# Kernel optimization log

Hardware: AMD Instinct MI355X
Metric: run time of the kernel (lower is better)

The kernel has to match this reference:

```python
import jax, jax.numpy as jnp
import numpy as np

BBOX_STD_DEV = jnp.array([0.1, 0.1, 0.2, 0.2], dtype=jnp.float32)
MIN_CONF = 0.15          # hardcoded in source (tf.where(probs >= 0.15))
NMS_THR = 0.3            # config.DETECTION_NMS_THRESHOLD
MAX_INST = 100           # config.DETECTION_MAX_INSTANCES
B, N = 8, 2048


def apply_box_deltas(boxes, deltas):
    # boxes: [N,4] (y1,x1,y2,x2); deltas: [N,4] (dy,dx,log dh,log dw)
    h = boxes[:, 2] - boxes[:, 0]
    w = boxes[:, 3] - boxes[:, 1]
    cy = boxes[:, 0] + 0.5 * h + deltas[:, 0] * h
    cx = boxes[:, 1] + 0.5 * w + deltas[:, 1] * w
    h = h * jnp.exp(deltas[:, 2])
    w = w * jnp.exp(deltas[:, 3])
    y1 = cy - 0.5 * h
    x1 = cx - 0.5 * w
    return jnp.stack([y1, x1, y1 + h, x1 + w], axis=1)


def clip_boxes(boxes, window):
    wy1, wx1, wy2, wx2 = window[0], window[1], window[2], window[3]
    y1 = jnp.clip(boxes[:, 0], wy1, wy2)
    x1 = jnp.clip(boxes[:, 1], wx1, wx2)
    y2 = jnp.clip(boxes[:, 2], wy1, wy2)
    x2 = jnp.clip(boxes[:, 3], wx1, wx2)
    return jnp.stack([y1, x1, y2, x2], axis=1)


def pairwise_iou(boxes):
    # boxes: [N,4] -> iou: [N,N]
    y1, x1, y2, x2 = boxes[:, 0], boxes[:, 1], boxes[:, 2], boxes[:, 3]
    area = (y2 - y1) * (x2 - x1)
    iy1 = jnp.maximum(y1[:, None], y1[None, :])
    ix1 = jnp.maximum(x1[:, None], x1[None, :])
    iy2 = jnp.minimum(y2[:, None], y2[None, :])
    ix2 = jnp.minimum(x2[:, None], x2[None, :])
    inter = jnp.maximum(iy2 - iy1, 0.0) * jnp.maximum(ix2 - ix1, 0.0)
    union = area[:, None] + area[None, :] - inter
    return inter / (union + 1e-8)


def refine_one(rois_i, probs_i, deltas_i, window_i):
    scores = probs_i[:, 0]
    boxes = clip_boxes(apply_box_deltas(rois_i, deltas_i * BBOX_STD_DEV), window_i)
    valid = scores >= MIN_CONF  # confidence filter (mask instead of gather)

    # sort by score descending; greedy NMS over sorted order
    order = jnp.argsort(-scores)
    sb, ss, sv = boxes[order], scores[order], valid[order]
    iou = pairwise_iou(sb)  # [N,N]
    idx = jnp.arange(N)

    def step(kept, xs):
        i, row, v = xs
        suppressed = jnp.any(kept & (idx < i) & (row > NMS_THR))
        return kept.at[i].set(v & ~suppressed), None

    kept, _ = jax.lax.scan(step, jnp.zeros((N,), dtype=bool), (idx, iou, sv))

    # top-k kept by score (already sorted desc, so top_k over masked scores)
    masked = jnp.where(kept, ss, -jnp.inf)
    _, top_i = jax.lax.top_k(masked, MAX_INST)
    ok = kept[top_i]
    det = jnp.concatenate([sb[top_i], ss[top_i][:, None]], axis=1)  # [MAX_INST,5]
    return jnp.where(ok[:, None], det, 0.0)  # zero-pad slots past num kept


def setup_inputs() -> dict:
    key = jax.random.key(0)
    k1, k2, k3 = jax.random.split(key, 3)
    # well-formed normalized rois: y1<y2, x1<x2
    yy = jnp.sort(jax.random.uniform(k1, (B, N, 2)), axis=-1)
    xx = jnp.sort(jax.random.uniform(jax.random.fold_in(k1, 1), (B, N, 2)), axis=-1)
    rois = jnp.stack([yy[..., 0], xx[..., 0], yy[..., 1], xx[..., 1]], axis=-1)
    bbox_scores = jax.random.uniform(k2, (B, N, 1), dtype=jnp.float32)
    deltas = jax.random.normal(k3, (B, N, 4), dtype=jnp.float32) * 0.1
    window = jnp.tile(jnp.array([[0.02, 0.02, 0.98, 0.98]], dtype=jnp.float32), (B, 1))
    return {"rois": rois, "bbox_scores": bbox_scores, "deltas": deltas, "window": window}


def reference(rois, bbox_scores, deltas, window):
    # -> [B, MAX_INST, 5] (y1,x1,y2,x2,score), normalized coords, zero padded
    return jax.vmap(refine_one)(rois, bbox_scores, deltas, window)
```

## Files before the change

kernel.cpp:

```cpp
#include <hip/hip_runtime.h>
#include <math.h>

#define NBOX 2048
#define NBATCH 8
#define MAX_INST 100
#define MIN_CONF 0.15f
#define NMS_THR 0.3f
#define BLOCK 512
#define NWAVE (BLOCK / 64)

typedef unsigned long long ull;

__device__ inline float4 decode_box(float4 r, float4 d,
                                    float wy1, float wx1, float wy2, float wx2) {
    float h  = __fsub_rn(r.z, r.x);
    float w  = __fsub_rn(r.w, r.y);
    float dy = __fmul_rn(d.x, 0.1f);
    float dx = __fmul_rn(d.y, 0.1f);
    float dh = __fmul_rn(d.z, 0.2f);
    float dw = __fmul_rn(d.w, 0.2f);
    float cy = __fadd_rn(__fadd_rn(r.x, __fmul_rn(0.5f, h)), __fmul_rn(dy, h));
    float cx = __fadd_rn(__fadd_rn(r.y, __fmul_rn(0.5f, w)), __fmul_rn(dx, w));
    float h2 = __fmul_rn(h, expf(dh));
    float w2 = __fmul_rn(w, expf(dw));
    float y1 = __fsub_rn(cy, __fmul_rn(0.5f, h2));
    float x1 = __fsub_rn(cx, __fmul_rn(0.5f, w2));
    float y2 = __fadd_rn(y1, h2);
    float x2 = __fadd_rn(x1, w2);
    float4 b;
    b.x = fminf(fmaxf(y1, wy1), wy2);
    b.y = fminf(fmaxf(x1, wx1), wx2);
    b.z = fminf(fmaxf(y2, wy1), wy2);
    b.w = fminf(fmaxf(x2, wx1), wx2);
    return b;
}

__device__ inline float iou_pair(float4 a, float4 b) {
    float areaA = __fmul_rn(__fsub_rn(a.z, a.x), __fsub_rn(a.w, a.y));
    float areaB = __fmul_rn(__fsub_rn(b.z, b.x), __fsub_rn(b.w, b.y));
    float iy1 = fmaxf(a.x, b.x);
    float ix1 = fmaxf(a.y, b.y);
    float iy2 = fminf(a.z, b.z);
    float ix2 = fminf(a.w, b.w);
    float ih = fmaxf(__fsub_rn(iy2, iy1), 0.0f);
    float iw = fmaxf(__fsub_rn(ix2, ix1), 0.0f);
    float inter = __fmul_rn(ih, iw);
    float uni = __fadd_rn(__fsub_rn(__fadd_rn(areaA, areaB), inter), 1e-8f);
    return __fdiv_rn(inter, uni);
}

__device__ inline ull shfl_xor64(ull x, int d) {
    unsigned lo = (unsigned)x, hi = (unsigned)(x >> 32);
    lo = __shfl_xor(lo, d);
    hi = __shfl_xor(hi, d);
    return ((ull)hi << 32) | lo;
}

__device__ inline ull shfl64(ull x, int src) {
    unsigned lo = (unsigned)x, hi = (unsigned)(x >> 32);
    lo = __shfl(lo, src);
    hi = __shfl(hi, src);
    return ((ull)hi << 32) | lo;
}

__device__ inline void cmpsel(ull& a, ull& b, bool takeMinA) {
    ull mn = a < b ? a : b;
    ull mx = a < b ? b : a;
    a = takeMinA ? mn : mx;
    b = takeMinA ? mx : mn;
}

__global__ __launch_bounds__(BLOCK)
void detect_refine_kernel(const float* __restrict__ rois,
                          const float* __restrict__ scores_in,
                          const float* __restrict__ deltas,
                          const float* __restrict__ window,
                          float* __restrict__ out) {
    const int b    = blockIdx.x;
    const int tid  = threadIdx.x;
    const int lane = tid & 63;
    const int wid  = tid >> 6;

    __shared__ ull    keys[NBOX];
    __shared__ float4 sboxes[NBOX];
    __shared__ float  sscores[NBOX];
    __shared__ ull    masks[64];
    __shared__ ull    dead8[NWAVE];
    __shared__ float4 s_keptbox[MAX_INST];
    __shared__ int    s_keptslot[64];
    __shared__ int    s_m;
    __shared__ ull    s_alive;

    const float wy1 = window[b * 4 + 0];
    const float wx1 = window[b * 4 + 1];
    const float wy2 = window[b * 4 + 2];
    const float wx2 = window[b * 4 + 3];

    float* outb = out + (size_t)b * MAX_INST * 5;
    for (int i = tid; i < MAX_INST * 5; i += BLOCK) outb[i] = 0.0f;

    for (int e = tid; e < NBOX; e += BLOCK) {
        float4 r = ((const float4*)rois)[b * NBOX + e];
        float4 d = ((const float4*)deltas)[b * NBOX + e];
        float  s = scores_in[b * NBOX + e];
        sboxes[e]  = decode_box(r, d, wy1, wx1, wy2, wx2);
        sscores[e] = s;
    }

    const int e0 = tid * 4;
    ull v[4];
    {
        float4 sc = ((const float4*)(scores_in + (size_t)b * NBOX))[tid];
        float s4[4] = {sc.x, sc.y, sc.z, sc.w};
#pragma unroll
        for (int s = 0; s < 4; ++s) {
            unsigned u = __float_as_uint(s4[s]);
            u = (u & 0x80000000u) ? ~u : (u | 0x80000000u);
            v[s] = ((ull)(~u) << 32) | (unsigned)(e0 + s);
        }
    }

    for (unsigned k = 2; k <= NBOX; k <<= 1) {
        if (k >= 512) {
#pragma unroll
            for (int s = 0; s < 4; ++s) keys[e0 + s] = v[s];
            __syncthreads();
            for (unsigned j = k >> 1; j >= 256; j >>= 1) {
                for (int t = tid; t < NBOX / 2; t += BLOCK) {
                    int i = 2 * t - (t & (j - 1));
                    int p = i | j;
                    bool up = ((i & k) == 0);
                    ull a = keys[i], c = keys[p];
                    bool sw = up ? (a > c) : (a < c);
                    if (sw) { keys[i] = c; keys[p] = a; }
                }
                __syncthreads();
            }
#pragma unroll
            for (int s = 0; s < 4; ++s) v[s] = keys[e0 + s];
        }
        unsigned jstart = ((k >> 1) > 128u) ? 128u : (k >> 1);
        for (unsigned j = jstart; j >= 4; j >>= 1) {
            int d = (int)(j >> 2);
#pragma unroll
            for (int s = 0; s < 4; ++s) {
                ull p = shfl_xor64(v[s], d);
                int e = e0 + s;
                bool takeMin = (((e & j) == 0) == ((e & k) == 0));
                v[s] = takeMin ? (v[s] < p ? v[s] : p) : (v[s] > p ? v[s] : p);
            }
        }
        if (k >= 4) {
            bool up = ((e0 & k) == 0);
            cmpsel(v[0], v[2], up);
            cmpsel(v[1], v[3], up);
        }
        {
            bool upA = ((e0 & k) == 0);
            bool upB = (((e0 + 2) & k) == 0);
            cmpsel(v[0], v[1], upA);
            cmpsel(v[2], v[3], upB);
        }
    }
#pragma unroll
    for (int s = 0; s < 4; ++s) keys[e0 + s] = v[s];
    __syncthreads();

    int count = 0;
    for (int cursor = 0; cursor < NBOX && count < MAX_INST; cursor += 64) {
        int   oi_j = (int)(keys[cursor + lane] & 0xFFFFFFFFull);
        float4 bj  = sboxes[oi_j];
        float  sj  = sscores[oi_j];

        bool deadp = (sj < MIN_CONF);
        for (int kk = wid; kk < count; kk += NWAVE)
            deadp |= (iou_pair(s_keptbox[kk], bj) > NMS_THR);
        ull bal = __ballot(deadp);
        if (lane == 0) dead8[wid] = bal;

        for (int i = wid; i < 64; i += NWAVE) {
            int   oi_i = (int)(keys[cursor + i] & 0xFFFFFFFFull);
            float4 bi  = sboxes[oi_i];
            bool pred  = (lane > i) && (iou_pair(bi, bj) > NMS_THR);
            ull  m     = __ballot(pred);
            if (lane == 0) masks[i] = m;
        }
        __syncthreads();

        if (wid == 0) {
            ull dead = dead8[0];
#pragma unroll
            for (int w = 1; w < NWAVE; ++w) dead |= dead8[w];
            ull alive = ~dead;
            ull mymask = masks[lane];
            int m = 0;
            const int maxm = MAX_INST - count;
            while (alive && m < maxm) {
                int i = __builtin_ctzll(alive);
                if (lane == 0) s_keptslot[m] = cursor + i;
                ++m;
                ull mi = shfl64(mymask, i);
                alive = alive & ~mi & ~(1ull << i);
            }
            if (lane == 0) s_m = m;
        }
        __syncthreads();

        const int m = s_m;
        if (tid < m) {
            int slot = s_keptslot[tid];
            int oi   = (int)(keys[slot] & 0xFFFFFFFFull);
            float4 bb = sboxes[oi];
            s_keptbox[count + tid] = bb;
            float* o = outb + (size_t)(count + tid) * 5;
            o[0] = bb.x; o[1] = bb.y; o[2] = bb.z; o[3] = bb.w;
            o[4] = sscores[oi];
        }
        count += m;
        __syncthreads();
    }
}

extern "C" void kernel_launch(void* const* d_in, const int* in_sizes, int n_in,
                              void* d_out, int out_size, void* d_ws, size_t ws_size,
                              hipStream_t stream) {
    const float* rois    = (const float*)d_in[0];
    const float* scores  = (const float*)d_in[1];
    const float* deltas  = (const float*)d_in[2];
    const float* window  = (const float*)d_in[3];
    float* out = (float*)d_out;
    detect_refine_kernel<<<NBATCH, BLOCK, 0, stream>>>(rois, scores, deltas, window, out);
}
```

Measured before the change: 48.90 us.

## Compact surviving candidates and prune them after each NMS window

Builds a compacted list of boxes that pass the confidence filter. NMS then runs over windows of 64 surviving candidates instead of fixed 64-slot chunks of the sorted order. After each window, every remaining candidate is tested only against the boxes just kept and the survivors are recompacted with ballot plus prefix offsets. This is meant to cut iterations spent on suppressed or low-score boxes, at the cost of extra compaction passes and barriers each round.

```diff
diff --git a/kernel.cpp b/kernel.cpp
--- a/kernel.cpp
+++ b/kernel.cpp
@@ -84,12 +84,15 @@
     __shared__ ull    keys[NBOX];
     __shared__ float4 sboxes[NBOX];
     __shared__ float  sscores[NBOX];
+    __shared__ int    aliveIdx[NBOX];
     __shared__ ull    masks[64];
-    __shared__ ull    dead8[NWAVE];
+    __shared__ ull    s_chunkMask[32];
+    __shared__ int    s_chunkCnt[32];
+    __shared__ int    s_chunkOff[32];
+    __shared__ int    s_aliveCount;
     __shared__ float4 s_keptbox[MAX_INST];
     __shared__ int    s_keptslot[64];
     __shared__ int    s_m;
-    __shared__ ull    s_alive;
 
     const float wy1 = window[b * 4 + 0];
     const float wx1 = window[b * 4 + 1];
@@ -166,38 +169,54 @@
     for (int s = 0; s < 4; ++s) keys[e0 + s] = v[s];
     __syncthreads();
 
+#pragma unroll
+    for (int r = 0; r < 4; ++r) {
+        int c = wid + r * NWAVE;
+        int oi = (int)(keys[c * 64 + lane] & 0xFFFFFFFFull);
+        bool alive = (sscores[oi] >= MIN_CONF);
+        ull bal = __ballot(alive);
+        if (lane == 0) { s_chunkMask[c] = bal; s_chunkCnt[c] = __popcll(bal); }
+    }
+    __syncthreads();
+    if (tid == 0) {
+        int acc = 0;
+        for (int c = 0; c < 32; ++c) { s_chunkOff[c] = acc; acc += s_chunkCnt[c]; }
+        s_aliveCount = acc;
+    }
+    __syncthreads();
+#pragma unroll
+    for (int r = 0; r < 4; ++r) {
+        int c = wid + r * NWAVE;
+        int oi = (int)(keys[c * 64 + lane] & 0xFFFFFFFFull);
+        ull msk = s_chunkMask[c];
+        if ((msk >> lane) & 1ull)
+            aliveIdx[s_chunkOff[c] + __popcll(msk & ((1ull << lane) - 1ull))] = oi;
+    }
+    __syncthreads();
+
+    int A = s_aliveCount;
     int count = 0;
-    for (int cursor = 0; cursor < NBOX && count < MAX_INST; cursor += 64) {
-        int   oi_j = (int)(keys[cursor + lane] & 0xFFFFFFFFull);
-        float4 bj  = sboxes[oi_j];
-        float  sj  = sscores[oi_j];
-
-        bool deadp = (sj < MIN_CONF);
-        for (int kk = wid; kk < count; kk += NWAVE)
-            deadp |= (iou_pair(s_keptbox[kk], bj) > NMS_THR);
-        ull bal = __ballot(deadp);
-        if (lane == 0) dead8[wid] = bal;
-
-        for (int i = wid; i < 64; i += NWAVE) {
-            int   oi_i = (int)(keys[cursor + i] & 0xFFFFFFFFull);
-            float4 bi  = sboxes[oi_i];
-            bool pred  = (lane > i) && (iou_pair(bi, bj) > NMS_THR);
-            ull  m     = __ballot(pred);
-            if (lane == 0) masks[i] = m;
+    while (A > 0 && count < MAX_INST) {
+        const int W = (A < 64) ? A : 64;
+
+        int    cj = (lane < W) ? aliveIdx[lane] : aliveIdx[0];
+        float4 bj = sboxes[cj];
+        for (int i = wid; i < W; i += NWAVE) {
+            float4 bi = sboxes[aliveIdx[i]];
+            bool pred = (lane > i) && (lane < W) && (iou_pair(bi, bj) > NMS_THR);
+            ull mrow = __ballot(pred);
+            if (lane == 0) masks[i] = mrow;
         }
         __syncthreads();
 
         if (wid == 0) {
-            ull dead = dead8[0];
-#pragma unroll
-            for (int w = 1; w < NWAVE; ++w) dead |= dead8[w];
-            ull alive = ~dead;
-            ull mymask = masks[lane];
+            ull alive  = (W >= 64) ? ~0ull : ((1ull << W) - 1ull);
+            ull mymask = (lane < W) ? masks[lane] : 0ull;
             int m = 0;
             const int maxm = MAX_INST - count;
             while (alive && m < maxm) {
                 int i = __builtin_ctzll(alive);
-                if (lane == 0) s_keptslot[m] = cursor + i;
+                if (lane == 0) s_keptslot[m] = i;
                 ++m;
                 ull mi = shfl64(mymask, i);
                 alive = alive & ~mi & ~(1ull << i);
@@ -208,16 +227,57 @@
 
         const int m = s_m;
         if (tid < m) {
-            int slot = s_keptslot[tid];
-            int oi   = (int)(keys[slot] & 0xFFFFFFFFull);
+            int oi = aliveIdx[s_keptslot[tid]];
             float4 bb = sboxes[oi];
             s_keptbox[count + tid] = bb;
             float* o = outb + (size_t)(count + tid) * 5;
             o[0] = bb.x; o[1] = bb.y; o[2] = bb.z; o[3] = bb.w;
             o[4] = sscores[oi];
         }
+        const int T = A - W;
         count += m;
-        __syncthreads();
+        if (count >= MAX_INST || T == 0) break;
+        __syncthreads();
+
+        const int nch = (T + 63) >> 6;
+        int  myval[4];
+        bool mykeep[4];
+#pragma unroll
+        for (int r = 0; r < 4; ++r) {
+            int c = wid + r * NWAVE;
+            bool keep = false; int val = 0;
+            if (c < nch) {
+                int e = 64 + c * 64 + lane;
+                if (e < A) {
+                    val = aliveIdx[e];
+                    float4 cb = sboxes[val];
+                    bool sup = false;
+                    for (int kk = count - m; kk < count; ++kk)
+                        sup |= (iou_pair(s_keptbox[kk], cb) > NMS_THR);
+                    keep = !sup;
+                }
+                ull bal = __ballot(keep);
+                if (lane == 0) { s_chunkMask[c] = bal; s_chunkCnt[c] = __popcll(bal); }
+            }
+            myval[r] = val; mykeep[r] = keep;
+        }
+        __syncthreads();
+        if (tid == 0) {
+            int acc = 0;
+            for (int c = 0; c < nch; ++c) { s_chunkOff[c] = acc; acc += s_chunkCnt[c]; }
+            s_aliveCount = acc;
+        }
+        __syncthreads();
+#pragma unroll
+        for (int r = 0; r < 4; ++r) {
+            int c = wid + r * NWAVE;
+            if (c < nch && mykeep[r]) {
+                ull msk = s_chunkMask[c];
+                aliveIdx[s_chunkOff[c] + __popcll(msk & ((1ull << lane) - 1ull))] = myval[r];
+            }
+        }
+        __syncthreads();
+        A = s_aliveCount;
     }
 }
 
```

Result: slower. 74.16 us (+51.6%).

## Widen NMS candidate window to 256 boxes with chunked suppression masks

Applied to the files above, without the earlier changes.

The greedy NMS loop now handles 256 sorted candidates per iteration instead of 64. Each window is staged into shared memory first, and a 256x256 upper-triangular IoU bitmask is built as four 64-bit chunks per row. Wave 0 then resolves the window serially using a cross-lane minimum over the four chunk bitmaps. This cuts the number of outer iterations and block barriers, but every window pays for a full 256x256 mask build even when only a few boxes are needed, and each serial step now costs more shuffle work.

```diff
diff --git a/kernel.cpp b/kernel.cpp
--- a/kernel.cpp
+++ b/kernel.cpp
@@ -7,7 +7,9 @@
 #define MIN_CONF 0.15f
 #define NMS_THR 0.3f
 #define BLOCK 512
-#define NWAVE (BLOCK / 64)
+#define NWAVE 8
+#define WIN 256
+#define NCH 4
 
 typedef unsigned long long ull;
 
@@ -56,13 +58,6 @@
     return ((ull)hi << 32) | lo;
 }
 
-__device__ inline ull shfl64(ull x, int src) {
-    unsigned lo = (unsigned)x, hi = (unsigned)(x >> 32);
-    lo = __shfl(lo, src);
-    hi = __shfl(hi, src);
-    return ((ull)hi << 32) | lo;
-}
-
 __device__ inline void cmpsel(ull& a, ull& b, bool takeMinA) {
     ull mn = a < b ? a : b;
     ull mx = a < b ? b : a;
@@ -84,12 +79,14 @@
     __shared__ ull    keys[NBOX];
     __shared__ float4 sboxes[NBOX];
     __shared__ float  sscores[NBOX];
-    __shared__ ull    masks[64];
-    __shared__ ull    dead8[NWAVE];
+    __shared__ float4 cbox[WIN];
+    __shared__ float  cscore[WIN];
+    __shared__ ull    s_masks[WIN][NCH];
+    __shared__ ull    s_aliveInit[NCH];
+    __shared__ ull    s_dead2[NCH][2];
     __shared__ float4 s_keptbox[MAX_INST];
-    __shared__ int    s_keptslot[64];
+    __shared__ int    s_kslot[MAX_INST];
     __shared__ int    s_m;
-    __shared__ ull    s_alive;
 
     const float wy1 = window[b * 4 + 0];
     const float wx1 = window[b * 4 + 1];
@@ -167,40 +164,62 @@
     __syncthreads();
 
     int count = 0;
-    for (int cursor = 0; cursor < NBOX && count < MAX_INST; cursor += 64) {
-        int   oi_j = (int)(keys[cursor + lane] & 0xFFFFFFFFull);
-        float4 bj  = sboxes[oi_j];
-        float  sj  = sscores[oi_j];
-
-        bool deadp = (sj < MIN_CONF);
-        for (int kk = wid; kk < count; kk += NWAVE)
-            deadp |= (iou_pair(s_keptbox[kk], bj) > NMS_THR);
-        ull bal = __ballot(deadp);
-        if (lane == 0) dead8[wid] = bal;
-
-        for (int i = wid; i < 64; i += NWAVE) {
-            int   oi_i = (int)(keys[cursor + i] & 0xFFFFFFFFull);
-            float4 bi  = sboxes[oi_i];
-            bool pred  = (lane > i) && (iou_pair(bi, bj) > NMS_THR);
-            ull  m     = __ballot(pred);
-            if (lane == 0) masks[i] = m;
+    for (int base = 0; base < NBOX && count < MAX_INST; base += WIN) {
+        if (tid < WIN) {
+            int oi = (int)(keys[base + tid] & 0xFFFFFFFFull);
+            float4 bb = sboxes[oi];
+            float  ss = sscores[oi];
+            cbox[tid]   = bb;
+            cscore[tid] = ss;
+            ull bal = __ballot(ss >= MIN_CONF);
+            if (lane == 0) s_aliveInit[wid] = bal;
+        }
+        __syncthreads();
+
+        {
+            const int g = wid >> 1, sub = wid & 1;
+            float4 myc = cbox[(g << 6) + lane];
+            bool deadp = false;
+            for (int k = sub; k < count; k += 2)
+                deadp |= (iou_pair(s_keptbox[k], myc) > NMS_THR);
+            ull bal = __ballot(deadp);
+            if (lane == 0) s_dead2[g][sub] = bal;
+        }
+        for (int i = wid; i < WIN; i += NWAVE) {
+            float4 bi = cbox[i];
+#pragma unroll
+            for (int q = 0; q < NCH; ++q) {
+                ull mrow = 0;
+                if ((q << 6) + 63 > i) {
+                    int col = (q << 6) + lane;
+                    bool pred = (col > i) && (iou_pair(bi, cbox[col]) > NMS_THR);
+                    mrow = __ballot(pred);
+                }
+                if (lane == 0) s_masks[i][q] = mrow;
+            }
         }
         __syncthreads();
 
         if (wid == 0) {
-            ull dead = dead8[0];
-#pragma unroll
-            for (int w = 1; w < NWAVE; ++w) dead |= dead8[w];
-            ull alive = ~dead;
-            ull mymask = masks[lane];
+            ull aliveL = 0;
+            if (lane < NCH)
+                aliveL = s_aliveInit[lane] & ~(s_dead2[lane][0] | s_dead2[lane][1]);
             int m = 0;
             const int maxm = MAX_INST - count;
-            while (alive && m < maxm) {
-                int i = __builtin_ctzll(alive);
-                if (lane == 0) s_keptslot[m] = cursor + i;
+            while (m < maxm) {
+                int pos = (lane < NCH && aliveL)
+                            ? ((lane << 6) + __builtin_ctzll(aliveL)) : WIN;
+                pos = min(pos, __shfl_xor(pos, 1));
+                pos = min(pos, __shfl_xor(pos, 2));
+                pos = __shfl(pos, 0);
+                if (pos >= WIN) break;
+                if (lane == 0) s_kslot[m] = pos;
                 ++m;
-                ull mi = shfl64(mymask, i);
-                alive = alive & ~mi & ~(1ull << i);
+                if (lane < NCH) {
+                    ull row = s_masks[pos][lane];
+                    if (lane == (pos >> 6)) row |= (1ull << (pos & 63));
+                    aliveL &= ~row;
+                }
             }
             if (lane == 0) s_m = m;
         }
@@ -208,13 +227,12 @@
 
         const int m = s_m;
         if (tid < m) {
-            int slot = s_keptslot[tid];
-            int oi   = (int)(keys[slot] & 0xFFFFFFFFull);
-            float4 bb = sboxes[oi];
+            int slot = s_kslot[tid];
+            float4 bb = cbox[slot];
             s_keptbox[count + tid] = bb;
             float* o = outb + (size_t)(count + tid) * 5;
             o[0] = bb.x; o[1] = bb.y; o[2] = bb.z; o[3] = bb.w;
-            o[4] = sscores[oi];
+            o[4] = cscore[slot];
         }
         count += m;
         __syncthreads();
```

Result: slower. 89.37 us (+82.8%).

## Compute intra-chunk suppression lazily in wave 0 and write output once at end

Applied to the files above, without the earlier changes.

Drops the precomputed 64x64 pairwise IoU mask matrix for each chunk. Wave 0 now tests the IoU of each newly kept box against the chunk with a ballot, so IoU work scales with the number of kept boxes instead of all pairs. Kept boxes and scores are broadcast by shuffle and staged in shared memory, and the output (with zero padding) is written once in a single coalesced pass at the end. This also removes one barrier per chunk. The trade-off is that the greedy loop is serialised on one wave, with an IoU per kept box where before there was only a mask lookup.

```diff
diff --git a/kernel.cpp b/kernel.cpp
--- a/kernel.cpp
+++ b/kernel.cpp
@@ -7,7 +7,7 @@
 #define MIN_CONF 0.15f
 #define NMS_THR 0.3f
 #define BLOCK 512
-#define NWAVE (BLOCK / 64)
+#define NWAVE 8
 
 typedef unsigned long long ull;
 
@@ -56,13 +56,6 @@
     return ((ull)hi << 32) | lo;
 }
 
-__device__ inline ull shfl64(ull x, int src) {
-    unsigned lo = (unsigned)x, hi = (unsigned)(x >> 32);
-    lo = __shfl(lo, src);
-    hi = __shfl(hi, src);
-    return ((ull)hi << 32) | lo;
-}
-
 __device__ inline void cmpsel(ull& a, ull& b, bool takeMinA) {
     ull mn = a < b ? a : b;
     ull mx = a < b ? b : a;
@@ -84,12 +77,10 @@
     __shared__ ull    keys[NBOX];
     __shared__ float4 sboxes[NBOX];
     __shared__ float  sscores[NBOX];
-    __shared__ ull    masks[64];
     __shared__ ull    dead8[NWAVE];
     __shared__ float4 s_keptbox[MAX_INST];
-    __shared__ int    s_keptslot[64];
+    __shared__ float  s_keptscore[MAX_INST];
     __shared__ int    s_m;
-    __shared__ ull    s_alive;
 
     const float wy1 = window[b * 4 + 0];
     const float wx1 = window[b * 4 + 1];
@@ -97,7 +88,6 @@
     const float wx2 = window[b * 4 + 3];
 
     float* outb = out + (size_t)b * MAX_INST * 5;
-    for (int i = tid; i < MAX_INST * 5; i += BLOCK) outb[i] = 0.0f;
 
     for (int e = tid; e < NBOX; e += BLOCK) {
         float4 r = ((const float4*)rois)[b * NBOX + e];
@@ -167,57 +157,60 @@
     __syncthreads();
 
     int count = 0;
-    for (int cursor = 0; cursor < NBOX && count < MAX_INST; cursor += 64) {
-        int   oi_j = (int)(keys[cursor + lane] & 0xFFFFFFFFull);
-        float4 bj  = sboxes[oi_j];
-        float  sj  = sscores[oi_j];
+    for (int base = 0; base < NBOX && count < MAX_INST; base += 64) {
+        int    oi = (int)(keys[base + lane] & 0xFFFFFFFFull);
+        float4 bj = sboxes[oi];
+        float  sj = sscores[oi];
 
         bool deadp = (sj < MIN_CONF);
-        for (int kk = wid; kk < count; kk += NWAVE)
-            deadp |= (iou_pair(s_keptbox[kk], bj) > NMS_THR);
+        for (int k = wid; k < count; k += NWAVE)
+            deadp |= (iou_pair(s_keptbox[k], bj) > NMS_THR);
         ull bal = __ballot(deadp);
         if (lane == 0) dead8[wid] = bal;
-
-        for (int i = wid; i < 64; i += NWAVE) {
-            int   oi_i = (int)(keys[cursor + i] & 0xFFFFFFFFull);
-            float4 bi  = sboxes[oi_i];
-            bool pred  = (lane > i) && (iou_pair(bi, bj) > NMS_THR);
-            ull  m     = __ballot(pred);
-            if (lane == 0) masks[i] = m;
-        }
         __syncthreads();
 
         if (wid == 0) {
             ull dead = dead8[0];
 #pragma unroll
-            for (int w = 1; w < NWAVE; ++w) dead |= dead8[w];
+            for (int w2 = 1; w2 < NWAVE; ++w2) dead |= dead8[w2];
             ull alive = ~dead;
-            ull mymask = masks[lane];
             int m = 0;
             const int maxm = MAX_INST - count;
             while (alive && m < maxm) {
                 int i = __builtin_ctzll(alive);
-                if (lane == 0) s_keptslot[m] = cursor + i;
+                float4 kb;
+                kb.x = __shfl(bj.x, i);
+                kb.y = __shfl(bj.y, i);
+                kb.z = __shfl(bj.z, i);
+                kb.w = __shfl(bj.w, i);
+                float ks = __shfl(sj, i);
+                if (lane == 0) {
+                    s_keptbox[count + m]   = kb;
+                    s_keptscore[count + m] = ks;
+                }
                 ++m;
-                ull mi = shfl64(mymask, i);
-                alive = alive & ~mi & ~(1ull << i);
+                ull sup = __ballot(iou_pair(kb, bj) > NMS_THR);
+                alive &= ~sup;
+                alive &= ~(1ull << i);
             }
             if (lane == 0) s_m = m;
         }
         __syncthreads();
-
-        const int m = s_m;
-        if (tid < m) {
-            int slot = s_keptslot[tid];
-            int oi   = (int)(keys[slot] & 0xFFFFFFFFull);
-            float4 bb = sboxes[oi];
-            s_keptbox[count + tid] = bb;
-            float* o = outb + (size_t)(count + tid) * 5;
-            o[0] = bb.x; o[1] = bb.y; o[2] = bb.z; o[3] = bb.w;
-            o[4] = sscores[oi];
-        }
-        count += m;
-        __syncthreads();
+        count += s_m;
+    }
+
+    for (int i = tid; i < MAX_INST * 5; i += BLOCK) {
+        int r = i / 5, c = i % 5;
+        float vout = 0.0f;
+        if (r < count) {
+            float4 bb = s_keptbox[r];
+            vout = (c == 0) ? bb.x
+                 : (c == 1) ? bb.y
+                 : (c == 2) ? bb.z
+                 : (c == 3) ? bb.w
+                 :            s_keptscore[r];
+        }
+        outb[i] = vout;
     }
 }
 
```

New measurement: 47.05 us. 1.04x faster.
